# Kernel optimization log

Hardware: AMD Instinct MI355X
Metric: run time of the kernel (lower is better)

The kernel has to match this reference:

```python
import jax, jax.numpy as jnp
import numpy as np

B, T, D = 256, 512, 128   # batch, T_max, input_dim
Z, TR, EM, RH = 128, 256, 256, 512  # z_dim, trans_dim, emission_dim, rnn_dim


def _dkf_infer(x, y, eps_comb, eps_emit, rnn_Wih, rnn_Whh, rnn_bih, rnn_bhh, h0, zq0,
               tr_g1_W, tr_g1_b, tr_g2_W, tr_g2_b, tr_p1_W, tr_p1_b, tr_p2_W, tr_p2_b,
               tr_mu_W, tr_mu_b, tr_lv_W, tr_lv_b,
               cb_h_W, cb_h_b, cb_mu_W, cb_mu_b, cb_lv_W, cb_lv_b,
               em_h1_W, em_h1_b, em_h2_W, em_h2_b, em_mu_W, em_mu_b, em_logvar):
    b = x.shape[0]
    # --- nn.RNN (relu nonlinearity, batch_first), scanned time-major ---
    xw = jnp.einsum('btd,dh->tbh', x, rnn_Wih) + rnn_bih  # [T,B,RH] input projection hoisted out of scan

    def rnn_step(h, xw_t):
        h = jax.nn.relu(xw_t + h @ rnn_Whh + rnn_bhh)
        return h, h

    _, rnn_out = jax.lax.scan(rnn_step, jnp.broadcast_to(h0, (b, h0.shape[0])), xw)  # [T,B,RH]

    y_tm = jnp.swapaxes(y, 0, 1)  # [T,B,D]

    def step(z_prev, inp):
        h_rnn, yt, e_cb, e_em = inp
        # GatedTransition (infer only uses prior mu/logvar; its sample is discarded)
        gate = jax.nn.sigmoid(jax.nn.relu(z_prev @ tr_g1_W + tr_g1_b) @ tr_g2_W + tr_g2_b)
        prop = jax.nn.relu(z_prev @ tr_p1_W + tr_p1_b) @ tr_p2_W + tr_p2_b
        pr_mu = (1.0 - gate) * (z_prev @ tr_mu_W + tr_mu_b) + gate * prop
        pr_lv = jax.nn.relu(prop) @ tr_lv_W + tr_lv_b
        # Combiner + reparameterization
        hc = 0.5 * (jnp.tanh(z_prev @ cb_h_W + cb_h_b) + h_rnn)
        mu = hc @ cb_mu_W + cb_mu_b
        lv = hc @ cb_lv_W + cb_lv_b
        z_t = mu + e_cb * jnp.exp(0.5 * lv)
        # Emitter + reparameterization
        h1 = jax.nn.relu(z_t @ em_h1_W + em_h1_b)
        h2 = jax.nn.relu(h1 @ em_h2_W + em_h2_b)
        x_mu = h2 @ em_mu_W + em_mu_b
        x_t = x_mu + e_em * jnp.exp(0.5 * em_logvar)
        # KL(q || prior) summed over z, per batch element
        kl = jnp.sum(0.5 * (pr_lv - lv + (jnp.exp(lv) + (mu - pr_mu) ** 2) / jnp.exp(pr_lv) - 1.0), axis=1)
        # per-element MSE reduced over x_dim
        rec = jnp.mean((x_t - yt) ** 2, axis=1)
        return z_t, (kl, rec)

    z0 = jnp.broadcast_to(zq0, (b, zq0.shape[0]))
    _, (kl_states, rec_losses) = jax.lax.scan(step, z0, (rnn_out, y_tm, eps_comb, eps_emit))
    return jnp.stack([jnp.mean(rec_losses), jnp.mean(kl_states)])  # [rec_loss, kl_loss]


def setup_inputs() -> dict:
    key = jax.random.key(0)
    ks = iter(jax.random.split(key, 32))
    nrm = lambda shape, s=0.05: jax.random.normal(next(ks), shape, dtype=jnp.float32) * s
    z = lambda *shape: jnp.zeros(shape, jnp.float32)
    return dict(
        x=nrm((B, T, D), 1.0), y=nrm((B, T, D), 1.0),
        eps_comb=nrm((T, B, Z), 1.0), eps_emit=nrm((T, B, D), 1.0),
        rnn_Wih=nrm((D, RH)), rnn_Whh=nrm((RH, RH)), rnn_bih=z(RH), rnn_bhh=z(RH),
        h0=z(RH), zq0=z(Z),
        tr_g1_W=nrm((Z, TR)), tr_g1_b=z(TR), tr_g2_W=nrm((TR, Z)), tr_g2_b=z(Z),
        tr_p1_W=nrm((Z, TR)), tr_p1_b=z(TR), tr_p2_W=nrm((TR, Z)), tr_p2_b=z(Z),
        tr_mu_W=jnp.eye(Z, dtype=jnp.float32), tr_mu_b=z(Z),  # identity init as in torch code
        tr_lv_W=nrm((Z, Z)), tr_lv_b=z(Z),
        cb_h_W=nrm((Z, RH)), cb_h_b=z(RH),
        cb_mu_W=nrm((RH, Z)), cb_mu_b=z(Z),
        cb_lv_W=nrm((RH, Z)), cb_lv_b=z(Z),
        em_h1_W=nrm((Z, EM)), em_h1_b=z(EM),
        em_h2_W=nrm((EM, EM)), em_h2_b=z(EM),
        em_mu_W=nrm((EM, D)), em_mu_b=z(D),
        em_logvar=jnp.ones((D,), jnp.float32),  # nn.Parameter(torch.ones(input_dim))
    )


def reference(x, y, eps_comb, eps_emit, rnn_Wih, rnn_Whh, rnn_bih, rnn_bhh, h0, zq0,
              tr_g1_W, tr_g1_b, tr_g2_W, tr_g2_b, tr_p1_W, tr_p1_b, tr_p2_W, tr_p2_b,
              tr_mu_W, tr_mu_b, tr_lv_W, tr_lv_b,
              cb_h_W, cb_h_b, cb_mu_W, cb_mu_b, cb_lv_W, cb_lv_b,
              em_h1_W, em_h1_b, em_h2_W, em_h2_b, em_mu_W, em_mu_b, em_logvar):
    return _dkf_infer(x, y, eps_comb, eps_emit, rnn_Wih, rnn_Whh, rnn_bih, rnn_bhh, h0, zq0,
                      tr_g1_W, tr_g1_b, tr_g2_W, tr_g2_b, tr_p1_W, tr_p1_b, tr_p2_W, tr_p2_b,
                      tr_mu_W, tr_mu_b, tr_lv_W, tr_lv_b,
                      cb_h_W, cb_h_b, cb_mu_W, cb_mu_b, cb_lv_W, cb_lv_b,
                      em_h1_W, em_h1_b, em_h2_W, em_h2_b, em_mu_W, em_mu_b, em_logvar)
```

## Files before the change

kernel.cpp:

```cpp
#include <hip/hip_runtime.h>


#define T_LEN 512
#define BATCH 256
#define DIMX  128
#define ZDIM  128
#define RHD   512
#define CHUNK 32

typedef _Float16 f16;
typedef _Float16 f16x4 __attribute__((ext_vector_type(4)));
typedef _Float16 f16x8 __attribute__((ext_vector_type(8)));
typedef float    f32x4 __attribute__((ext_vector_type(4)));

#define MFMA16(a,b,c) __builtin_amdgcn_mfma_f32_16x16x32_f16((a),(b),(c),0,0,0)

#define PK_WIH  0u
#define PK_WHH  65536u
#define PK_G1   327680u
#define PK_G2   360448u
#define PK_P1   393216u
#define PK_P2   425984u
#define PK_TMU  458752u
#define PK_TLV  475136u
#define PK_CBH  491520u
#define PK_CBML 557056u
#define PK_E1   688128u
#define PK_E2   720896u
#define PK_EMU  786432u

#define WS_XW   0ull
#define WS_Z    (WS_XW  + 134217728ull)
#define WS_MU   (WS_Z   + 33619968ull)
#define WS_LV   (WS_MU  + 33554432ull)
#define WS_PK   (WS_LV  + 33554432ull)
#define WS_PART (WS_PK  + 1638400ull)
#define WS_PROG (WS_PART + 16384ull)
#define WS_END  (WS_PROG + 256ull)

__device__ __forceinline__ void ldsfence() {
  asm volatile("s_waitcnt lgkmcnt(0)" ::: "memory");
  __builtin_amdgcn_sched_barrier(0);
}

__device__ __forceinline__ void lbar() {
  asm volatile("s_waitcnt lgkmcnt(0)" ::: "memory");
  __builtin_amdgcn_s_barrier();
  asm volatile("" ::: "memory");
}

__device__ __forceinline__ void pin8(f16x8& v) {
  f32x4 t = __builtin_bit_cast(f32x4, v);
  asm volatile("" : "+v"(t));
  v = __builtin_bit_cast(f16x8, t);
}

template<int N>
__device__ __forceinline__ void zacc(f32x4* a) {
  f32x4 z = {0.f, 0.f, 0.f, 0.f};
#pragma unroll
  for (int i = 0; i < N; ++i) a[i] = z;
}

__device__ __forceinline__ f16x8 cvt8(const float* p) {
  float4 a = *(const float4*)p, b = *(const float4*)(p + 4);
  f16x8 r;
  r[0] = (f16)a.x; r[1] = (f16)a.y; r[2] = (f16)a.z; r[3] = (f16)a.w;
  r[4] = (f16)b.x; r[5] = (f16)b.y; r[6] = (f16)b.z; r[7] = (f16)b.w;
  return r;
}

__device__ __forceinline__ int swz(int row, int col) {
  return (row << 9) + (col ^ ((row & 7) << 3));
}
__device__ __forceinline__ int swz128(int row, int col) {
  return (row << 7) + (col ^ ((row & 7) << 3));
}

template<int KS>
__device__ __forceinline__ void load_af(const f16* src, int sstr, int lane, f16x8* af) {
#pragma unroll
  for (int ks = 0; ks < KS; ++ks)
    af[ks] = *(const f16x8*)(src + (lane & 15) * sstr + ks * 32 + ((lane >> 4) << 3));
}

template<int KS, int NT>
__device__ __forceinline__ void gemm_regA(const f16x8* af, const f16* __restrict__ bp,
                                          int lane, f32x4* acc) {
#pragma unroll
  for (int ks = 0; ks < KS; ++ks)
#pragma unroll
    for (int j = 0; j < NT; ++j) {
      f16x8 bf = *(const f16x8*)(bp + (((size_t)(ks * NT + j)) << 9) + (lane << 3));
      acc[j] = MFMA16(af[ks], bf, acc[j]);
    }
}

template<int NT>
__device__ __forceinline__ void store_relu(const f32x4* acc, const float* __restrict__ bias,
                                           f16* dst, int dstr, int lane) {
  int colv = lane & 15, rb = (lane >> 4) << 2;
#pragma unroll
  for (int j = 0; j < NT; ++j)
#pragma unroll
    for (int r = 0; r < 4; ++r)
      dst[(rb + r) * dstr + j * 16 + colv] = (f16)fmaxf(acc[j][r] + bias[j * 16 + colv], 0.f);
}

__device__ __forceinline__ unsigned ldflag(const unsigned* p) {
  return __hip_atomic_load(p, __ATOMIC_RELAXED, __HIP_MEMORY_SCOPE_AGENT);
}

struct PackEnt { const float* s1; const float* s2; int nsplit, K, N; unsigned dst, wg0; };
struct PackTab { PackEnt e[13]; };

__global__ void pack_all_kernel(PackTab tb, f16* __restrict__ pk) {
  int i = 0;
#pragma unroll
  for (int k = 1; k < 13; ++k)
    if (blockIdx.x >= tb.e[k].wg0) i = k;
  const PackEnt& E = tb.e[i];
  int idx = (blockIdx.x - E.wg0) * 256 + threadIdx.x;
  if (idx >= E.K * E.N) return;
  int j = idx & 7, l = (idx >> 3) & 63, fi = idx >> 9;
  int NTt = E.N >> 4;
  int nt = fi % NTt, ks = fi / NTt;
  int k = ks * 32 + ((l >> 4) << 3) + j;
  int n = (nt << 4) + (l & 15);
  float v;
  if (n < E.nsplit) v = E.s1[(size_t)k * E.nsplit + n];
  else              v = E.s2[(size_t)k * (E.N - E.nsplit) + (n - E.nsplit)];
  pk[E.dst + idx] = (f16)v;
}

__global__ void zero_prog_kernel(unsigned* __restrict__ p) {
  if (threadIdx.x < 64)
    __hip_atomic_store(p + threadIdx.x, 0u, __ATOMIC_RELAXED, __HIP_MEMORY_SCOPE_AGENT);
}

__global__ __launch_bounds__(512, 2) void scan_pipe_kernel(
    const f16* __restrict__ pk, const float* __restrict__ h0,
    const float* __restrict__ zq0, const float* __restrict__ chb,
    const float* __restrict__ cmb, const float* __restrict__ clb,
    const float* __restrict__ eps_comb, f16* __restrict__ xw,
    f16* __restrict__ z_all, f16* __restrict__ mu_all, f16* __restrict__ lv_all,
    const float* __restrict__ x, const float* __restrict__ bih,
    const float* __restrict__ bhh, unsigned* __restrict__ flags) {
  __shared__ __align__(16) f16 lds[73728];
  const int tid = threadIdx.x, lane = tid & 63, w = tid >> 6;
  const int colv = lane & 15, l4 = lane >> 4;
  unsigned* prog = flags;
  unsigned* xcnt = flags + 32;

  if (blockIdx.x < 16) {
    const int g = blockIdx.x, b0 = g * 16;
    f16* whh_lds = lds;
    f16* h_st = lds + 65536;
    {
      const uint4* src = (const uint4*)(pk + PK_WHH + 196608u);
      for (int i = tid; i < 8192; i += 512) ((uint4*)whh_lds)[i] = src[i];
    }
    f16x8 whhA[4][12];
#pragma unroll
    for (int mt = 0; mt < 4; ++mt)
#pragma unroll
      for (int ks = 0; ks < 12; ++ks) {
        whhA[mt][ks] = *(const f16x8*)(pk + PK_WHH +
            ((size_t)(ks * 32 + 4 * w + mt) << 9) + (lane << 3));
        pin8(whhA[mt][ks]);
      }
    for (int i = tid; i < 8192; i += 512) h_st[swz(i >> 9, i & 511)] = (f16)h0[i & 511];
    __syncthreads();

    if (tid == 0) { while (ldflag(xcnt + 0) < 64u) __builtin_amdgcn_s_sleep(2); }
    __syncthreads();
    __builtin_amdgcn_fence(__ATOMIC_ACQUIRE, "agent");

    const int off0 = (4 * w) * 16 + l4 * 4;
    f16* xp = xw + (size_t)(b0 + colv) * RHD;
    f16x4 xwc[4], xwn[4];
#pragma unroll
    for (int mt = 0; mt < 4; ++mt) xwc[mt] = *(const f16x4*)(xp + off0 + mt * 16);

    for (int c = 0; c < T_LEN / CHUNK; ++c) {
      const int cw = (c + 1 < T_LEN / CHUNK) ? c + 1 : T_LEN / CHUNK - 1;
      if (tid == 0) { while (ldflag(xcnt + cw) < 64u) __builtin_amdgcn_s_sleep(2); }
      __syncthreads();
      __builtin_amdgcn_fence(__ATOMIC_ACQUIRE, "agent");
#pragma unroll 1
      for (int tt = 0; tt < CHUNK; ++tt) {
        int t = c * CHUNK + tt;
        f16* xpn = (t < T_LEN - 1) ? xp + (size_t)BATCH * RHD : xp;
#pragma unroll
        for (int mt = 0; mt < 4; ++mt) xwn[mt] = *(const f16x4*)(xpn + off0 + mt * 16);

        f32x4 acc[4]; zacc<4>(acc);
#pragma unroll
        for (int kc = 0; kc < 6; ++kc) {
          f16x8 B2[2];
#pragma unroll
          for (int kk = 0; kk < 2; ++kk)
            B2[kk] = *(const f16x8*)&h_st[swz(colv, (kc * 2 + kk) * 32 + l4 * 8)];
#pragma unroll
          for (int kk = 0; kk < 2; ++kk)
#pragma unroll
            for (int mt = 0; mt < 4; ++mt)
              acc[mt] = MFMA16(whhA[mt][kc * 2 + kk], B2[kk], acc[mt]);
        }
#pragma unroll
        for (int kc = 0; kc < 2; ++kc) {
          f16x8 B2[2];
#pragma unroll
          for (int kk = 0; kk < 2; ++kk)
            B2[kk] = *(const f16x8*)&h_st[swz(colv, (12 + kc * 2 + kk) * 32 + l4 * 8)];
#pragma unroll
          for (int kk = 0; kk < 2; ++kk)
#pragma unroll
            for (int mt = 0; mt < 4; ++mt)
              acc[mt] = MFMA16(*(const f16x8*)(whh_lds +
                  ((((kc * 2 + kk) * 32 + 4 * w + mt) << 6) + lane) * 8), B2[kk], acc[mt]);
        }
        lbar();
#pragma unroll
        for (int mt = 0; mt < 4; ++mt) {
          f16x4 h4;
#pragma unroll
          for (int r = 0; r < 4; ++r)
            h4[r] = (f16)fmaxf(acc[mt][r] + (float)xwc[mt][r], 0.f);
          *(f16x4*)&h_st[swz(colv, off0 + mt * 16)] = h4;
          *(f16x4*)(xp + off0 + mt * 16) = h4;
        }
        lbar();
        xp = xpn;
#pragma unroll
        for (int mt = 0; mt < 4; ++mt) xwc[mt] = xwn[mt];
      }
      __syncthreads();
      if (tid == 0)
        __hip_atomic_store(prog + g, (unsigned)(c + 1), __ATOMIC_RELEASE,
                           __HIP_MEMORY_SCOPE_AGENT);
    }
  } else if (blockIdx.x < 32) {
    const int g = blockIdx.x - 16, b0 = g * 16;
    f16* cbml_lds = lds;
    f16* hc_st = lds + 32768;
    f16* z_st  = lds + 40960;
    f16* m_st  = lds + 43008;
    {
      const uint4* src = (const uint4*)(pk + PK_CBML + 98304u);
      for (int i = tid; i < 4096; i += 512) ((uint4*)cbml_lds)[i] = src[i];
    }
    f16x8 cbhA[4][4];
#pragma unroll
    for (int mt = 0; mt < 4; ++mt)
#pragma unroll
      for (int ks = 0; ks < 4; ++ks) {
        cbhA[mt][ks] = *(const f16x8*)(pk + PK_CBH +
            ((size_t)(ks * 32 + 4 * w + mt) << 9) + (lane << 3));
        pin8(cbhA[mt][ks]);
      }
    f16x8 cbmlA[2][12];
#pragma unroll
    for (int mt = 0; mt < 2; ++mt)
#pragma unroll
      for (int ks = 0; ks < 12; ++ks) {
        cbmlA[mt][ks] = *(const f16x8*)(pk + PK_CBML +
            ((size_t)(ks * 16 + 2 * w + mt) << 9) + (lane << 3));
        pin8(cbmlA[mt][ks]);
      }
    f16x4 chbv[4];
#pragma unroll
    for (int mt = 0; mt < 4; ++mt)
#pragma unroll
      for (int r = 0; r < 4; ++r)
        chbv[mt][r] = (f16)chb[(4 * w + mt) * 16 + l4 * 4 + r];
    float mb[2][4];
#pragma unroll
    for (int mt = 0; mt < 2; ++mt)
#pragma unroll
      for (int r = 0; r < 4; ++r) {
        int d = (2 * w + mt) * 16 + l4 * 4 + r;
        mb[mt][r] = (d < 128) ? cmb[d] : clb[d - 128];
      }
    for (int i = tid; i < 2048; i += 512) {
      f16 zv = (f16)zq0[i & 127];
      z_st[swz128(i >> 7, i & 127)] = zv;
      z_all[(size_t)(b0 + (i >> 7)) * ZDIM + (i & 127)] = zv;
    }
    __syncthreads();

    const int hoff = (4 * w) * 16 + l4 * 4;
    const int be = tid >> 5, d0 = (tid & 31) * 4;
    const f16* hp = xw + (size_t)(b0 + colv) * RHD;
    const float* epb = eps_comb + (size_t)(b0 + be) * ZDIM + d0;
    f16x4 hvc[4], hvn[4];

    for (int c = 0; c < T_LEN / CHUNK; ++c) {
      if (tid == 0) {
        while (ldflag(prog + g) < (unsigned)(c + 1)) __builtin_amdgcn_s_sleep(2);
      }
      __syncthreads();
      __builtin_amdgcn_fence(__ATOMIC_ACQUIRE, "agent");
      {
        const f16* hpt = hp + (size_t)(c * CHUNK) * BATCH * RHD;
#pragma unroll
        for (int mt = 0; mt < 4; ++mt) hvc[mt] = *(const f16x4*)(hpt + hoff + mt * 16);
      }
#pragma unroll 1
      for (int tt = 0; tt < CHUNK; ++tt) {
        int t = c * CHUNK + tt;
        float4 ep = *(const float4*)(epb + (size_t)t * BATCH * ZDIM);

        f16x8 zB[4];
#pragma unroll
        for (int ks = 0; ks < 4; ++ks)
          zB[ks] = *(const f16x8*)&z_st[swz128(colv, ks * 32 + l4 * 8)];
        f32x4 a1[4]; zacc<4>(a1);
#pragma unroll
        for (int ks = 0; ks < 4; ++ks)
#pragma unroll
          for (int mt = 0; mt < 4; ++mt)
            a1[mt] = MFMA16(cbhA[mt][ks], zB[ks], a1[mt]);
#pragma unroll
        for (int mt = 0; mt < 4; ++mt) {
          f16x4 hc4;
#pragma unroll
          for (int r = 0; r < 4; ++r) {
            float cs = a1[mt][r] + (float)chbv[mt][r];
            float ex = __builtin_amdgcn_exp2f(cs * 2.885390082f);
            float th = 1.f - 2.f * __builtin_amdgcn_rcpf(ex + 1.f);
            hc4[r] = (f16)(0.5f * (th + (float)hvc[mt][r]));
          }
          *(f16x4*)&hc_st[swz(colv, hoff + mt * 16)] = hc4;
        }
        lbar();
        if (tt < CHUNK - 1) {
          const f16* hpt = hp + (size_t)(t + 1) * BATCH * RHD;
#pragma unroll
          for (int mt = 0; mt < 4; ++mt) hvn[mt] = *(const f16x4*)(hpt + hoff + mt * 16);
        }
        f32x4 a2[2]; zacc<2>(a2);
#pragma unroll
        for (int kc = 0; kc < 6; ++kc) {
          f16x8 hcB[2];
#pragma unroll
          for (int kk = 0; kk < 2; ++kk)
            hcB[kk] = *(const f16x8*)&hc_st[swz(colv, (kc * 2 + kk) * 32 + l4 * 8)];
#pragma unroll
          for (int kk = 0; kk < 2; ++kk)
#pragma unroll
            for (int mt = 0; mt < 2; ++mt)
              a2[mt] = MFMA16(cbmlA[mt][kc * 2 + kk], hcB[kk], a2[mt]);
        }
#pragma unroll
        for (int kc = 0; kc < 2; ++kc) {
          f16x8 hcB[2];
#pragma unroll
          for (int kk = 0; kk < 2; ++kk)
            hcB[kk] = *(const f16x8*)&hc_st[swz(colv, (12 + kc * 2 + kk) * 32 + l4 * 8)];
#pragma unroll
          for (int kk = 0; kk < 2; ++kk)
#pragma unroll
            for (int mt = 0; mt < 2; ++mt)
              a2[mt] = MFMA16(*(const f16x8*)(cbml_lds +
                  ((((kc * 2 + kk) * 16 + 2 * w + mt) << 6) + lane) * 8), hcB[kk], a2[mt]);
        }
#pragma unroll
        for (int mt = 0; mt < 2; ++mt) {
          f16x4 v;
#pragma unroll
          for (int r = 0; r < 4; ++r) v[r] = (f16)(a2[mt][r] + mb[mt][r]);
          *(f16x4*)&m_st[colv * 264 + (2 * w + mt) * 16 + l4 * 4] = v;
        }
        lbar();
        {
          f16x4 muf = *(const f16x4*)&m_st[be * 264 + d0];
          f16x4 lvf = *(const f16x4*)&m_st[be * 264 + 128 + d0];
          float epv[4] = {ep.x, ep.y, ep.z, ep.w};
          f16x4 z4;
#pragma unroll
          for (int r = 0; r < 4; ++r) {
            float mu = (float)muf[r], lv = (float)lvf[r];
            z4[r] = (f16)(mu + epv[r] * __builtin_amdgcn_exp2f(lv * 0.7213475204f));
          }
          *(f16x4*)&z_st[swz128(be, d0)] = z4;
          size_t o = ((size_t)t * BATCH + b0 + be) * ZDIM + d0;
          *(f16x4*)(z_all + o + (size_t)BATCH * ZDIM) = z4;
          *(f16x4*)(mu_all + o) = muf;
          *(f16x4*)(lv_all + o) = lvf;
        }
        lbar();
#pragma unroll
        for (int mt = 0; mt < 4; ++mt) hvc[mt] = hvn[mt];
      }
    }
  } else {
    const int p = blockIdx.x - 32;
    float* bs = (float*)lds;
    for (int i = tid; i < 512; i += 512) bs[i] = bih[i] + bhh[i];
    if (tid < 512) { int i2 = tid; bs[i2] = bih[i2] + bhh[i2]; }
    __syncthreads();
    for (int c = 0; c < T_LEN / CHUNK; ++c) {
      if (c > 2) {
        if (tid == 0) {
          for (;;) {
            unsigned mn = 0xffffffffu;
            for (int g2 = 0; g2 < 16; ++g2) mn = min(mn, ldflag(prog + g2));
            if (mn >= (unsigned)(c - 2)) break;
            __builtin_amdgcn_s_sleep(32);
          }
        }
        __syncthreads();
      }
#pragma unroll 1
      for (int q = 0; q < 2; ++q) {
        const int i = c * 64 + p * 2 + q;
        const int m0 = i * 128 + w * 16;
        const int t = m0 >> 8, b0 = m0 & 255;
        f16x8 xB[4];
        const float* xr = x + ((size_t)(b0 + colv) * T_LEN + t) * DIMX;
#pragma unroll
        for (int ks = 0; ks < 4; ++ks) xB[ks] = cvt8(xr + ks * 32 + l4 * 8);
        f32x4 acc[32]; zacc<32>(acc);
#pragma unroll
        for (int ks = 0; ks < 4; ++ks)
#pragma unroll
          for (int mt = 0; mt < 32; ++mt)
            acc[mt] = MFMA16(*(const f16x8*)(pk + PK_WIH +
                ((size_t)(ks * 32 + mt) << 9) + (lane << 3)), xB[ks], acc[mt]);
        f16* xo = xw + ((size_t)t * BATCH + b0 + colv) * RHD;
#pragma unroll
        for (int mt = 0; mt < 32; ++mt) {
          f16x4 v;
#pragma unroll
          for (int r = 0; r < 4; ++r) v[r] = (f16)(acc[mt][r] + bs[mt * 16 + l4 * 4 + r]);
          *(f16x4*)(xo + mt * 16 + l4 * 4) = v;
        }
        __syncthreads();
        if (tid == 0)
          __hip_atomic_fetch_add(xcnt + c, 1u, __ATOMIC_RELEASE,
                                 __HIP_MEMORY_SCOPE_AGENT);
      }
    }
  }
}

__global__ __launch_bounds__(256) void dpar_kernel(
    const f16* __restrict__ z_all, const f16* __restrict__ mu_all,
    const f16* __restrict__ lv_all, const float* __restrict__ y,
    const float* __restrict__ eps_emit, const f16* __restrict__ pk,
    const float* __restrict__ g1b, const float* __restrict__ g2b,
    const float* __restrict__ p1b, const float* __restrict__ p2b,
    const float* __restrict__ tmub, const float* __restrict__ tlvb,
    const float* __restrict__ e1b, const float* __restrict__ e2b,
    const float* __restrict__ emub, const float* __restrict__ em_logvar,
    float* __restrict__ partials) {
  __shared__ __align__(16) f16 sb256[4][16 * 264];
  __shared__ __align__(16) f16 sb128[4][16 * 136];
  __shared__ float wsum[4][2];
  const int tid = threadIdx.x, lane = tid & 63, w = tid >> 6;
  const int colv = lane & 15, rb = (lane >> 4) << 2;
  const int m0 = blockIdx.x * 64 + w * 16;
  const int t = m0 >> 8, b0 = m0 & 255;
  f16* B256 = &sb256[w][0];
  f16* B128 = &sb128[w][0];

  f16x8 zp[4], zt[4];
  const f16* zpr = z_all + ((size_t)t * BATCH + b0) * ZDIM;
#pragma unroll
  for (int ks = 0; ks < 4; ++ks) {
    zp[ks] = *(const f16x8*)(zpr + (size_t)colv * ZDIM + ks * 32 + ((lane >> 4) << 3));
    zt[ks] = *(const f16x8*)(zpr + (size_t)BATCH * ZDIM + (size_t)colv * ZDIM + ks * 32 + ((lane >> 4) << 3));
  }

  f32x4 a16[16], a8[8];
  f16x8 af[8], af4[4];
  zacc<16>(a16); gemm_regA<4, 16>(zp, pk + PK_G1, lane, a16);
  store_relu<16>(a16, g1b, B256, 264, lane); ldsfence();
  load_af<8>(B256, 264, lane, af); ldsfence();
  zacc<8>(a8); gemm_regA<8, 8>(af, pk + PK_G2, lane, a8);
  f32x4 gate[8];
#pragma unroll
  for (int j = 0; j < 8; ++j)
#pragma unroll
    for (int r = 0; r < 4; ++r)
      gate[j][r] = 1.f / (1.f + expf(-(a8[j][r] + g2b[j * 16 + colv])));
  zacc<16>(a16); gemm_regA<4, 16>(zp, pk + PK_P1, lane, a16);
  store_relu<16>(a16, p1b, B256, 264, lane); ldsfence();
  load_af<8>(B256, 264, lane, af); ldsfence();
  zacc<8>(a8); gemm_regA<8, 8>(af, pk + PK_P2, lane, a8);
  f32x4 prop[8];
#pragma unroll
  for (int j = 0; j < 8; ++j)
#pragma unroll
    for (int r = 0; r < 4; ++r) {
      float v = a8[j][r] + p2b[j * 16 + colv];
      prop[j][r] = v;
      B128[(rb + r) * 136 + j * 16 + colv] = (f16)fmaxf(v, 0.f);
    }
  ldsfence();
  zacc<8>(a8); gemm_regA<4, 8>(zp, pk + PK_TMU, lane, a8);
  f32x4 prmu[8];
#pragma unroll
  for (int j = 0; j < 8; ++j)
#pragma unroll
    for (int r = 0; r < 4; ++r) {
      float gg = gate[j][r];
      prmu[j][r] = (1.f - gg) * (a8[j][r] + tmub[j * 16 + colv]) + gg * prop[j][r];
    }
  load_af<4>(B128, 136, lane, af4); ldsfence();
  zacc<8>(a8); gemm_regA<4, 8>(af4, pk + PK_TLV, lane, a8);
  f32x4 prlv[8];
#pragma unroll
  for (int j = 0; j < 8; ++j)
#pragma unroll
    for (int r = 0; r < 4; ++r) prlv[j][r] = a8[j][r] + tlvb[j * 16 + colv];
  zacc<16>(a16); gemm_regA<4, 16>(zt, pk + PK_E1, lane, a16);
  store_relu<16>(a16, e1b, B256, 264, lane); ldsfence();
  load_af<8>(B256, 264, lane, af); ldsfence();
  zacc<16>(a16); gemm_regA<8, 16>(af, pk + PK_E2, lane, a16);
  store_relu<16>(a16, e2b, B256, 264, lane); ldsfence();
  load_af<8>(B256, 264, lane, af); ldsfence();
  zacc<8>(a8); gemm_regA<8, 8>(af, pk + PK_EMU, lane, a8);
  float srec = 0.f, skl = 0.f;
#pragma unroll
  for (int j = 0; j < 8; ++j)
#pragma unroll
    for (int r = 0; r < 4; ++r) {
      int row = rb + r, n = j * 16 + colv;
      size_t tb = (size_t)t * BATCH + b0 + row;
      float xt = a8[j][r] + emub[n] + eps_emit[tb * DIMX + n] * expf(0.5f * em_logvar[n]);
      float dy = xt - y[((size_t)(b0 + row) * T_LEN + t) * DIMX + n];
      srec += dy * dy;
      float m_ = (float)mu_all[tb * ZDIM + n], l_ = (float)lv_all[tb * ZDIM + n];
      float dm = m_ - prmu[j][r];
      skl += 0.5f * (prlv[j][r] - l_ + (expf(l_) + dm * dm) * expf(-prlv[j][r]) - 1.f);
    }
#pragma unroll
  for (int off = 32; off; off >>= 1) {
    srec += __shfl_xor(srec, off);
    skl += __shfl_xor(skl, off);
  }
  if (lane == 0) { wsum[w][0] = srec; wsum[w][1] = skl; }
  __syncthreads();
  if (tid == 0) {
    partials[blockIdx.x * 2 + 0] = wsum[0][0] + wsum[1][0] + wsum[2][0] + wsum[3][0];
    partials[blockIdx.x * 2 + 1] = wsum[0][1] + wsum[1][1] + wsum[2][1] + wsum[3][1];
  }
}

__global__ void finalize_kernel(const float* __restrict__ partials, float* __restrict__ out) {
  __shared__ float sm[256][2];
  int tid = threadIdx.x;
  float r = 0.f, kk = 0.f;
  for (int i = tid; i < 2048; i += 256) {
    r += partials[2 * i];
    kk += partials[2 * i + 1];
  }
  sm[tid][0] = r; sm[tid][1] = kk;
  __syncthreads();
  for (int off = 128; off; off >>= 1) {
    if (tid < off) { sm[tid][0] += sm[tid + off][0]; sm[tid][1] += sm[tid + off][1]; }
    __syncthreads();
  }
  if (tid == 0) {
    out[0] = sm[0][0] / (131072.f * 128.f);
    out[1] = sm[0][1] / 131072.f;
  }
}

extern "C" void kernel_launch(void* const* d_in, const int* in_sizes, int n_in,
                              void* d_out, int out_size, void* d_ws, size_t ws_size,
                              hipStream_t stream) {
  (void)in_sizes; (void)n_in; (void)out_size;
  const float* x        = (const float*)d_in[0];
  const float* y        = (const float*)d_in[1];
  const float* eps_comb = (const float*)d_in[2];
  const float* eps_emit = (const float*)d_in[3];
  const float* wih = (const float*)d_in[4];
  const float* whh = (const float*)d_in[5];
  const float* bih = (const float*)d_in[6];
  const float* bhh = (const float*)d_in[7];
  const float* h0  = (const float*)d_in[8];
  const float* zq0 = (const float*)d_in[9];
  const float* g1W = (const float*)d_in[10]; const float* g1b = (const float*)d_in[11];
  const float* g2W = (const float*)d_in[12]; const float* g2b = (const float*)d_in[13];
  const float* p1W = (const float*)d_in[14]; const float* p1b = (const float*)d_in[15];
  const float* p2W = (const float*)d_in[16]; const float* p2b = (const float*)d_in[17];
  const float* tmuW = (const float*)d_in[18]; const float* tmub = (const float*)d_in[19];
  const float* tlvW = (const float*)d_in[20]; const float* tlvb = (const float*)d_in[21];
  const float* chW = (const float*)d_in[22]; const float* chb = (const float*)d_in[23];
  const float* cmW = (const float*)d_in[24]; const float* cmb = (const float*)d_in[25];
  const float* clW = (const float*)d_in[26]; const float* clb = (const float*)d_in[27];
  const float* e1W = (const float*)d_in[28]; const float* e1b = (const float*)d_in[29];
  const float* e2W = (const float*)d_in[30]; const float* e2b = (const float*)d_in[31];
  const float* emW = (const float*)d_in[32]; const float* emb = (const float*)d_in[33];
  const float* elv = (const float*)d_in[34];

  char* ws = (char*)d_ws;
  f16*  xw      = (f16*)(ws + WS_XW);
  f16*  z_all   = (f16*)(ws + WS_Z);
  f16*  mu_all  = (f16*)(ws + WS_MU);
  f16*  lv_all  = (f16*)(ws + WS_LV);
  f16*  pk      = (f16*)(ws + WS_PK);
  float* partials = (float*)(ws + WS_PART);
  unsigned* flags = (unsigned*)(ws + WS_PROG);
  float* out = (float*)d_out;
  if (ws_size < WS_END) return;

  zero_prog_kernel<<<dim3(1), dim3(64), 0, stream>>>(flags);

  PackTab tb;
  unsigned wg = 0; int ei = 0;
#define PACK(S1, S2, NS_, K_, N_, OFF) \
  tb.e[ei] = PackEnt{S1, S2, NS_, K_, N_, OFF, wg}; wg += (unsigned)((K_) * (N_)) / 256; ++ei;
  PACK(wih, wih, 512, 128, 512, PK_WIH);
  PACK(whh, whh, 512, 512, 512, PK_WHH);
  PACK(g1W, g1W, 256, 128, 256, PK_G1);
  PACK(g2W, g2W, 128, 256, 128, PK_G2);
  PACK(p1W, p1W, 256, 128, 256, PK_P1);
  PACK(p2W, p2W, 128, 256, 128, PK_P2);
  PACK(tmuW, tmuW, 128, 128, 128, PK_TMU);
  PACK(tlvW, tlvW, 128, 128, 128, PK_TLV);
  PACK(chW, chW, 512, 128, 512, PK_CBH);
  PACK(cmW, clW, 128, 512, 256, PK_CBML);
  PACK(e1W, e1W, 256, 128, 256, PK_E1);
  PACK(e2W, e2W, 256, 256, 256, PK_E2);
  PACK(emW, emW, 128, 256, 128, PK_EMU);
#undef PACK
  pack_all_kernel<<<dim3(wg), dim3(256), 0, stream>>>(tb, pk);

  scan_pipe_kernel<<<dim3(64), dim3(512), 0, stream>>>(
      pk, h0, zq0, chb, cmb, clb, eps_comb, xw, z_all, mu_all, lv_all,
      x, bih, bhh, flags);
  dpar_kernel<<<dim3(2048), dim3(256), 0, stream>>>(z_all, mu_all, lv_all, y, eps_emit, pk,
                                                    g1b, g2b, p1b, p2b, tmub, tlvb, e1b, e2b,
                                                    emb, elv, partials);
  finalize_kernel<<<dim3(1), dim3(256), 0, stream>>>(partials, out);
}
```

Measured before the change: 2.829 ms.

## Move RNN input projection out of the persistent scan into a separate kernel

Takes out the 32 producer workgroups that computed the x@Wih projection chunk by chunk inside the persistent scan kernel, along with the xcnt flag handshakes. The projection now runs up front as its own 2048-block kernel, and the scan kernel launches with only 32 blocks (RNN and combiner). This drops per-chunk spin-waits and lets the projection run wide across the whole GPU. In exchange it gives up overlapping the projection with the serial recurrence, so its time now sits before the scan on the critical path.

```diff
diff --git a/kernel.cpp b/kernel.cpp
--- a/kernel.cpp
+++ b/kernel.cpp
@@ -138,19 +138,48 @@
     __hip_atomic_store(p + threadIdx.x, 0u, __ATOMIC_RELAXED, __HIP_MEMORY_SCOPE_AGENT);
 }
 
+__global__ __launch_bounds__(256) void xw_kernel(
+    const float* __restrict__ x, const f16* __restrict__ pk,
+    const float* __restrict__ bih, const float* __restrict__ bhh,
+    f16* __restrict__ xw) {
+  __shared__ float bs[512];
+  const int tid = threadIdx.x, lane = tid & 63, w = tid >> 6;
+  const int colv = lane & 15, l4 = lane >> 4;
+  const int m0 = blockIdx.x * 64 + w * 16;
+  const int t = m0 >> 8, b0 = m0 & 255;
+  for (int i = tid; i < 512; i += 256) bs[i] = bih[i] + bhh[i];
+  __syncthreads();
+  f16x8 xB[4];
+  const float* xr = x + ((size_t)(b0 + colv) * T_LEN + t) * DIMX;
+#pragma unroll
+  for (int ks = 0; ks < 4; ++ks) xB[ks] = cvt8(xr + ks * 32 + l4 * 8);
+  f32x4 acc[32]; zacc<32>(acc);
+#pragma unroll
+  for (int ks = 0; ks < 4; ++ks)
+#pragma unroll
+    for (int mt = 0; mt < 32; ++mt)
+      acc[mt] = MFMA16(*(const f16x8*)(pk + PK_WIH + ((size_t)(ks * 32 + mt) << 9) + (lane << 3)),
+                       xB[ks], acc[mt]);
+  f16* xo = xw + ((size_t)t * BATCH + b0 + colv) * RHD;
+#pragma unroll
+  for (int mt = 0; mt < 32; ++mt) {
+    f16x4 v;
+#pragma unroll
+    for (int r = 0; r < 4; ++r) v[r] = (f16)(acc[mt][r] + bs[mt * 16 + l4 * 4 + r]);
+    *(f16x4*)(xo + mt * 16 + l4 * 4) = v;
+  }
+}
+
 __global__ __launch_bounds__(512, 2) void scan_pipe_kernel(
     const f16* __restrict__ pk, const float* __restrict__ h0,
     const float* __restrict__ zq0, const float* __restrict__ chb,
     const float* __restrict__ cmb, const float* __restrict__ clb,
     const float* __restrict__ eps_comb, f16* __restrict__ xw,
     f16* __restrict__ z_all, f16* __restrict__ mu_all, f16* __restrict__ lv_all,
-    const float* __restrict__ x, const float* __restrict__ bih,
-    const float* __restrict__ bhh, unsigned* __restrict__ flags) {
+    unsigned* __restrict__ prog) {
   __shared__ __align__(16) f16 lds[73728];
   const int tid = threadIdx.x, lane = tid & 63, w = tid >> 6;
   const int colv = lane & 15, l4 = lane >> 4;
-  unsigned* prog = flags;
-  unsigned* xcnt = flags + 32;
 
   if (blockIdx.x < 16) {
     const int g = blockIdx.x, b0 = g * 16;
@@ -172,10 +201,6 @@
     for (int i = tid; i < 8192; i += 512) h_st[swz(i >> 9, i & 511)] = (f16)h0[i & 511];
     __syncthreads();
 
-    if (tid == 0) { while (ldflag(xcnt + 0) < 64u) __builtin_amdgcn_s_sleep(2); }
-    __syncthreads();
-    __builtin_amdgcn_fence(__ATOMIC_ACQUIRE, "agent");
-
     const int off0 = (4 * w) * 16 + l4 * 4;
     f16* xp = xw + (size_t)(b0 + colv) * RHD;
     f16x4 xwc[4], xwn[4];
@@ -183,10 +208,6 @@
     for (int mt = 0; mt < 4; ++mt) xwc[mt] = *(const f16x4*)(xp + off0 + mt * 16);
 
     for (int c = 0; c < T_LEN / CHUNK; ++c) {
-      const int cw = (c + 1 < T_LEN / CHUNK) ? c + 1 : T_LEN / CHUNK - 1;
-      if (tid == 0) { while (ldflag(xcnt + cw) < 64u) __builtin_amdgcn_s_sleep(2); }
-      __syncthreads();
-      __builtin_amdgcn_fence(__ATOMIC_ACQUIRE, "agent");
 #pragma unroll 1
       for (int tt = 0; tt < CHUNK; ++tt) {
         int t = c * CHUNK + tt;
@@ -240,7 +261,7 @@
         __hip_atomic_store(prog + g, (unsigned)(c + 1), __ATOMIC_RELEASE,
                            __HIP_MEMORY_SCOPE_AGENT);
     }
-  } else if (blockIdx.x < 32) {
+  } else {
     const int g = blockIdx.x - 16, b0 = g * 16;
     f16* cbml_lds = lds;
     f16* hc_st = lds + 32768;
@@ -392,54 +413,6 @@
         lbar();
 #pragma unroll
         for (int mt = 0; mt < 4; ++mt) hvc[mt] = hvn[mt];
-      }
-    }
-  } else {
-    const int p = blockIdx.x - 32;
-    float* bs = (float*)lds;
-    for (int i = tid; i < 512; i += 512) bs[i] = bih[i] + bhh[i];
-    if (tid < 512) { int i2 = tid; bs[i2] = bih[i2] + bhh[i2]; }
-    __syncthreads();
-    for (int c = 0; c < T_LEN / CHUNK; ++c) {
-      if (c > 2) {
-        if (tid == 0) {
-          for (;;) {
-            unsigned mn = 0xffffffffu;
-            for (int g2 = 0; g2 < 16; ++g2) mn = min(mn, ldflag(prog + g2));
-            if (mn >= (unsigned)(c - 2)) break;
-            __builtin_amdgcn_s_sleep(32);
-          }
-        }
-        __syncthreads();
-      }
-#pragma unroll 1
-      for (int q = 0; q < 2; ++q) {
-        const int i = c * 64 + p * 2 + q;
-        const int m0 = i * 128 + w * 16;
-        const int t = m0 >> 8, b0 = m0 & 255;
-        f16x8 xB[4];
-        const float* xr = x + ((size_t)(b0 + colv) * T_LEN + t) * DIMX;
-#pragma unroll
-        for (int ks = 0; ks < 4; ++ks) xB[ks] = cvt8(xr + ks * 32 + l4 * 8);
-        f32x4 acc[32]; zacc<32>(acc);
-#pragma unroll
-        for (int ks = 0; ks < 4; ++ks)
-#pragma unroll
-          for (int mt = 0; mt < 32; ++mt)
-            acc[mt] = MFMA16(*(const f16x8*)(pk + PK_WIH +
-                ((size_t)(ks * 32 + mt) << 9) + (lane << 3)), xB[ks], acc[mt]);
-        f16* xo = xw + ((size_t)t * BATCH + b0 + colv) * RHD;
-#pragma unroll
-        for (int mt = 0; mt < 32; ++mt) {
-          f16x4 v;
-#pragma unroll
-          for (int r = 0; r < 4; ++r) v[r] = (f16)(acc[mt][r] + bs[mt * 16 + l4 * 4 + r]);
-          *(f16x4*)(xo + mt * 16 + l4 * 4) = v;
-        }
-        __syncthreads();
-        if (tid == 0)
-          __hip_atomic_fetch_add(xcnt + c, 1u, __ATOMIC_RELEASE,
-                                 __HIP_MEMORY_SCOPE_AGENT);
       }
     }
   }
@@ -604,11 +577,11 @@
   f16*  lv_all  = (f16*)(ws + WS_LV);
   f16*  pk      = (f16*)(ws + WS_PK);
   float* partials = (float*)(ws + WS_PART);
-  unsigned* flags = (unsigned*)(ws + WS_PROG);
+  unsigned* prog  = (unsigned*)(ws + WS_PROG);
   float* out = (float*)d_out;
   if (ws_size < WS_END) return;
 
-  zero_prog_kernel<<<dim3(1), dim3(64), 0, stream>>>(flags);
+  zero_prog_kernel<<<dim3(1), dim3(64), 0, stream>>>(prog);
 
   PackTab tb;
   unsigned wg = 0; int ei = 0;
@@ -630,9 +603,9 @@
 #undef PACK
   pack_all_kernel<<<dim3(wg), dim3(256), 0, stream>>>(tb, pk);
 
-  scan_pipe_kernel<<<dim3(64), dim3(512), 0, stream>>>(
-      pk, h0, zq0, chb, cmb, clb, eps_comb, xw, z_all, mu_all, lv_all,
-      x, bih, bhh, flags);
+  xw_kernel<<<dim3(2048), dim3(256), 0, stream>>>(x, pk, bih, bhh, xw);
+  scan_pipe_kernel<<<dim3(32), dim3(512), 0, stream>>>(
+      pk, h0, zq0, chb, cmb, clb, eps_comb, xw, z_all, mu_all, lv_all, prog);
   dpar_kernel<<<dim3(2048), dim3(256), 0, stream>>>(z_all, mu_all, lv_all, y, eps_emit, pk,
                                                     g1b, g2b, p1b, p2b, tmub, tlvb, e1b, e2b,
                                                     emb, elv, partials);
```

After: 2.826 ms. About the same (-0.1%).
